# Optimization experiments

Measured on AMD Instinct MI355X. Metric: run time of the kernel, lower is better.

## Reference

```python
import math
import jax, jax.numpy as jnp
import numpy as np

LOG2PI = math.log(2.0 * math.pi)


def setup_inputs() -> dict:
    key = jax.random.key(0)
    k1, k2, k3 = jax.random.split(key, 3)
    N, K, d, l = 16384, 32, 1024, 16
    x = jax.random.normal(k1, (N, d), dtype=jnp.float32)
    MU = jax.random.normal(k2, (K, d), dtype=jnp.float32)
    # modest factor-loading scale so A^T A + s2 I is well conditioned
    A = 0.1 * jax.random.normal(k3, (K, d, l), dtype=jnp.float32)
    log_D = jnp.zeros((K, d), dtype=jnp.float32)       # isotropic sigma^2 = 1
    PI_logits = jnp.zeros((K,), dtype=jnp.float32)     # uniform mixture
    return {"x": x, "MU": MU, "A": A, "log_D": log_D, "PI_logits": PI_logits}


def _responsibilities(x, MU, A, log_D, PI_logits):
    """E-step: faithful vectorization of MFA._component_log_likelihood + softmax.
    Note: the original adds PI (probabilities), not log PI -- kept as-is."""
    K, d, l = A.shape
    PI = jax.nn.softmax(PI_logits)
    iD = jnp.exp(-log_D)                                  # [K,d]
    B = iD[:, :, None] * A                                # iD * A, [K,d,l]
    L = jnp.eye(l, dtype=x.dtype)[None] + jnp.einsum('kdl,kdm->klm', A, B)  # [K,l,l]
    iL = jnp.linalg.inv(L)
    # Mahalanobis distance via Woodbury, without materializing [N,K,d]:
    # term1 = sum_d iD * x_c^2, expanded in x, MU
    sq = (x * x) @ iD.T                                   # [N,K]
    cross = x @ (iD * MU).T                               # [N,K]
    const = jnp.sum(iD * MU * MU, axis=1)                 # [K]
    term1 = sq - 2.0 * cross + const[None, :]
    # term2 = (iD x_c)^T A iL A^T (iD x_c)
    y = jnp.einsum('nd,kdl->nkl', x, B) - jnp.einsum('kd,kdl->kl', MU, B)[None]
    term2 = jnp.einsum('nkl,klm,nkm->nk', y, iL, y)
    m_d = term1 - term2                                   # [N,K]
    log_det_Sigma = jnp.linalg.slogdet(L)[1] - jnp.sum(jnp.log(iD), axis=1)
    comp_LL = PI[None, :] - 0.5 * ((d * LOG2PI + log_det_Sigma)[None, :] + m_d)
    log_r = comp_LL - jax.nn.logsumexp(comp_LL, axis=1, keepdims=True)
    return jnp.exp(log_r)


def reference(x, MU, A, log_D, PI_logits):
    """One EM iteration of MFA.fit: E-step + batched (over K) M-step.
    Returns (MU_new, A_new, log_D_new, PI_logits_new)."""
    K, d, l = A.shape
    r = _responsibilities(x, MU, A, log_D, PI_logits)     # [N,K]
    r_sum = jnp.sum(r, axis=0)                            # [K]
    mu_new = (r.T @ x) / r_sum[:, None]                   # [K,d]
    s2 = jnp.exp(log_D[:, 0])                             # [K]
    eye_l = jnp.eye(l, dtype=x.dtype)
    inv_M = jnp.linalg.inv(jnp.einsum('kdl,kdm->klm', A, A)
                           + s2[:, None, None] * eye_l)   # [K,l,l]
    # SiAi_k = (1/rs_k) * (r_k * x_c)^T @ (x_c @ A_k), expanded so only
    # [N,K,l] (not [N,K,d]) intermediates are built.
    Q = jnp.einsum('nd,kdl->nkl', x, A) - jnp.einsum('kd,kdl->kl', mu_new, A)[None]
    RQ = r[:, :, None] * Q                                # [N,K,l]
    sumRQ = jnp.sum(RQ, axis=0)                           # [K,l]
    SiAi = (jnp.einsum('nd,nkl->kdl', x, RQ)
            - mu_new[:, :, None] * sumRQ[:, None, :]) / r_sum[:, None, None]
    ATSiAi = jnp.einsum('kdl,kdm->klm', A, SiAi)          # [K,l,l]
    invM_AT_Si_Ai = jnp.einsum('klm,kmp->klp', inv_M, ATSiAi)
    A_new = jnp.einsum('kdm,kml->kdl', SiAi,
                       jnp.linalg.inv(s2[:, None, None] * eye_l + invM_AT_Si_Ai))
    SiAi_invM = jnp.einsum('kdm,kml->kdl', SiAi, inv_M)
    t1 = jnp.einsum('kdl,kdl->k', A_new, SiAi_invM)       # trace term
    # trace(S_i) = (sum_n r_nk ||x_n - mu_k||^2) / rs_k, expanded
    x_sq = jnp.sum(x * x, axis=1)                         # [N]
    trace_S = (r.T @ x_sq - r_sum * jnp.sum(mu_new * mu_new, axis=1)) / r_sum
    sigma2_new = (trace_S - t1) / d                       # [K]
    log_D_new = jnp.log(sigma2_new)[:, None] * jnp.ones((1, d), dtype=x.dtype)
    PI_logits_new = jnp.log(r_sum / jnp.sum(r_sum))
    return mu_new, A_new, log_D_new, PI_logits_new
```

## Files before the change

### kernel.cpp

```cpp
#include <hip/hip_runtime.h>
#include <math.h>

#define N_ROWS 16384
#define DIM 1024
#define KC 32
#define LF 16
#define LOG2PI_F 1.8378770664093453f
#define Y_STRIDE 560

typedef __attribute__((ext_vector_type(8))) short bf16x8;
typedef __attribute__((ext_vector_type(4))) float f32x4;

#define O_XH    0
#define O_XL    8388608
#define O_RQT   O_XL
#define O_XBT   16777216
#define O_Y     25165824
#define O_SIAZ  O_Y
#define O_SQ    34340864
#define O_R     34865152
#define O_WETH  35389440
#define O_WETL  35667968
#define O_AQT   35946496
#define O_ID    36208640
#define O_SIAI  36241408
#define O_LMAT  36765696
#define O_M0    36773888
#define O_IL    36782080
#define O_INVM  36790272
#define O_GM    36798464
#define O_IG    36806656
#define O_CB    36814848
#define O_CA    36815360
#define O_CONST 36815872
#define O_SLD   36815904
#define O_LDET  36815936
#define O_PIK   36815968
#define O_CK    36816000
#define O_MUSQ  36816032
#define O_MUACC 36816064
#define O_SUMRQ 36848832
#define O_RSUM  36849344
#define O_RXSQ  36849376
#define O_T1    36849408
#define ZERO_START O_MUACC
#define ZERO_COUNT 33376
#define O_XSQ   36849440

#define OU_MU 0
#define OU_A  32768
#define OU_LD 557056
#define OU_PI 589824

__device__ __forceinline__ ushort f2bf(float f) {
    union { float f; unsigned u; } v; v.f = f;
    unsigned u = v.u;
    return (ushort)((u + 0x7FFFu + ((u >> 16) & 1u)) >> 16);
}
__device__ __forceinline__ float bf2f(ushort b) {
    union { unsigned u; float f; } v; v.u = ((unsigned)b) << 16;
    return v.f;
}

__device__ __forceinline__ float blockReduce256(float v, float* red) {
    int tid = threadIdx.x;
    red[tid] = v; __syncthreads();
    for (int s = 128; s > 0; s >>= 1) {
        if (tid < s) red[tid] += red[tid + s];
        __syncthreads();
    }
    float r = red[0]; __syncthreads();
    return r;
}

__global__ __launch_bounds__(256) void k_conv(const float* __restrict__ x,
    float* __restrict__ ws)
{
    __shared__ ushort tile[64][66];
    int tid = threadIdx.x;
    int n0 = blockIdx.x * 64;
    int row = tid >> 2, seg = tid & 3;
    ushort* xh  = (ushort*)(ws + O_XH);
    ushort* xl  = (ushort*)(ws + O_XL);
    ushort* xbT = (ushort*)(ws + O_XBT);

    for (int c0 = 0; c0 < DIM; c0 += 64) {
        float4 f[4];
        #pragma unroll
        for (int t = 0; t < 4; t++)
            f[t] = *(const float4*)&x[(size_t)(n0 + row)*DIM + c0 + seg*16 + t*4];
        union { ushort u[8]; uint4 v; } ha, hb, la, lb;
        ushort hi16[16];
        #pragma unroll
        for (int e = 0; e < 16; e++) {
            float v = ((const float*)&f[e >> 2])[e & 3];
            ushort h = f2bf(v);
            hi16[e] = h;
            ushort lo = f2bf(v - bf2f(h));
            if (e < 8) { ha.u[e] = h; la.u[e] = lo; }
            else       { hb.u[e-8] = h; lb.u[e-8] = lo; }
        }
        size_t o = (size_t)(n0 + row)*DIM + c0 + seg*16;
        *(uint4*)&xh[o] = ha.v;  *(uint4*)&xh[o + 8] = hb.v;
        *(uint4*)&xl[o] = la.v;  *(uint4*)&xl[o + 8] = lb.v;
        #pragma unroll
        for (int e = 0; e < 16; e++) tile[seg*16 + e][row] = hi16[e];
        __syncthreads();
        int cl = tid >> 2, nseg = tid & 3;
        union { ushort u[8]; uint4 v; } ta, tb;
        #pragma unroll
        for (int e = 0; e < 8; e++) {
            ta.u[e] = tile[cl][nseg*16 + e];
            tb.u[e] = tile[cl][nseg*16 + 8 + e];
        }
        size_t ot = (size_t)(c0 + cl)*N_ROWS + n0 + nseg*16;
        *(uint4*)&xbT[ot] = ta.v; *(uint4*)&xbT[ot + 8] = tb.v;
        __syncthreads();
    }
}

__global__ __launch_bounds__(256) void k_prep(
    const float* __restrict__ MU, const float* __restrict__ A,
    const float* __restrict__ logD, const float* __restrict__ PIl,
    float* __restrict__ ws)
{
    int k = blockIdx.x, tid = threadIdx.x;
    __shared__ float red[256];
    ushort* Weth = (ushort*)(ws + O_WETH);
    ushort* Wetl = (ushort*)(ws + O_WETL);
    ushort* Aqt  = (ushort*)(ws + O_AQT);
    float* iDb = ws + O_ID;

    float cb[LF];
    #pragma unroll
    for (int l = 0; l < LF; l++) cb[l] = 0.f;
    float cst = 0.f, sl = 0.f;

    for (int dd = tid; dd < DIM; dd += 256) {
        float ld  = logD[k*DIM + dd];
        float idv = expf(-ld);
        float mu  = MU[k*DIM + dd];
        cst += idv*mu*mu;
        sl  += ld;
        iDb[(size_t)k*DIM + dd] = idv;
        const float* arow = A + (size_t)(k*DIM + dd)*LF;
        #pragma unroll
        for (int l = 0; l < LF; l++) {
            float a = arow[l];
            float b = idv*a;
            ushort h = f2bf(b);
            Weth[(size_t)(k*LF + l)*DIM + dd] = h;
            Wetl[(size_t)(k*LF + l)*DIM + dd] = f2bf(b - bf2f(h));
            Aqt[(size_t)(k*LF + l)*DIM + dd] = f2bf(a);
            cb[l] += mu*b;
        }
        float cmu = idv*mu;
        ushort hm = f2bf(cmu);
        Weth[(size_t)(512 + k)*DIM + dd] = hm;
        Wetl[(size_t)(512 + k)*DIM + dd] = f2bf(cmu - bf2f(hm));
    }

    for (int l = 0; l < LF; l++) {
        float t = blockReduce256(cb[l], red);
        if (tid == 0) ws[O_CB + k*LF + l] = t;
    }
    {
        float t = blockReduce256(cst, red);
        if (tid == 0) ws[O_CONST + k] = t;
        t = blockReduce256(sl, red);
        if (tid == 0) ws[O_SLD + k] = t;
    }
    if (tid == 0) {
        float mx = -1e30f;
        for (int j = 0; j < KC; j++) mx = fmaxf(mx, PIl[j]);
        float s = 0.f;
        for (int j = 0; j < KC; j++) s += expf(PIl[j] - mx);
        ws[O_PIK + k] = expf(PIl[k] - mx) / s;
    }
    __syncthreads();

    int i = tid >> 4, j = tid & 15;
    float sL = 0.f, sM = 0.f;
    for (int dd = 0; dd < DIM; dd++) {
        const float* arow = A + (size_t)(k*DIM + dd)*LF;
        float ai = arow[i], aj = arow[j];
        float idv = iDb[(size_t)k*DIM + dd];
        sL += ai*aj*idv;
        sM += ai*aj;
    }
    float s2 = expf(logD[k*DIM]);
    ws[O_LMAT + k*256 + tid] = sL + (i == j ? 1.f : 0.f);
    ws[O_M0   + k*256 + tid] = sM + (i == j ? s2  : 0.f);
}

__global__ __launch_bounds__(256) void k_inv16(const float* __restrict__ src,
    float* __restrict__ dst, float* __restrict__ ldet)
{
    __shared__ float M[16][33];
    __shared__ float fac[16];
    __shared__ int spv;
    __shared__ float sld;
    int m = blockIdx.x, tid = threadIdx.x;

    for (int idx = tid; idx < 16*33; idx += 256) {
        int i = idx/33, c = idx%33;
        M[i][c] = (c < 16) ? src[m*256 + i*16 + c]
                           : (c < 32 ? ((i == c-16) ? 1.f : 0.f) : 0.f);
    }
    if (tid == 0) sld = 0.f;
    __syncthreads();

    for (int j = 0; j < 16; j++) {
        if (tid == 0) {
            int p = j; float best = fabsf(M[j][j]);
            for (int i2 = j+1; i2 < 16; i2++) {
                float a = fabsf(M[i2][j]);
                if (a > best) { best = a; p = i2; }
            }
            spv = p;
            sld += logf(fabsf(M[p][j]));
        }
        __syncthreads();
        int p = spv;
        if (p != j && tid < 33) { float t = M[j][tid]; M[j][tid] = M[p][tid]; M[p][tid] = t; }
        __syncthreads();
        float pv = M[j][j];
        __syncthreads();
        if (tid < 33) M[j][tid] = M[j][tid] / pv;
        __syncthreads();
        if (tid < 16) fac[tid] = M[tid][j];
        __syncthreads();
        for (int idx = tid; idx < 16*33; idx += 256) {
            int i2 = idx/33, c = idx%33;
            if (i2 != j) M[i2][c] -= fac[i2]*M[j][c];
        }
        __syncthreads();
    }
    {
        int i = tid >> 4, c = tid & 15;
        dst[m*256 + tid] = M[i][16 + c];
    }
    if (ldet != nullptr && tid == 0) ldet[m] = sld;
}

__global__ void k_prep2(float* __restrict__ ws)
{
    int k = threadIdx.x;
    if (k < KC) {
        ws[O_CK + k] = ws[O_PIK + k]
            - 0.5f*((float)DIM*LOG2PI_F + ws[O_LDET + k] + ws[O_SLD + k] + ws[O_CONST + k]);
    }
}

__global__ __launch_bounds__(256) void k_sq(const float* __restrict__ x,
    const float* __restrict__ iD, float* __restrict__ SQ, float* __restrict__ xsq)
{
    __shared__ float xs[32][65];
    __shared__ float ds[32][65];
    int tid = threadIdx.x;
    int n0 = blockIdx.x * 32;
    int r = tid & 31, ks = (tid >> 5) * 4;
    int srow = tid >> 3, sc = (tid & 7) * 8;
    float acc[4] = {0.f, 0.f, 0.f, 0.f};
    float xsa = 0.f;

    for (int d0 = 0; d0 < DIM; d0 += 64) {
        __syncthreads();
        #pragma unroll
        for (int u = 0; u < 8; u += 4) {
            float4 a = *(const float4*)&x[(size_t)(n0 + srow)*DIM + d0 + sc + u];
            xs[srow][sc+u+0] = a.x*a.x; xs[srow][sc+u+1] = a.y*a.y;
            xs[srow][sc+u+2] = a.z*a.z; xs[srow][sc+u+3] = a.w*a.w;
            float4 b = *(const float4*)&iD[(size_t)srow*DIM + d0 + sc + u];
            ds[srow][sc+u+0] = b.x; ds[srow][sc+u+1] = b.y;
            ds[srow][sc+u+2] = b.z; ds[srow][sc+u+3] = b.w;
        }
        __syncthreads();
        for (int d = 0; d < 64; d++) {
            float xv = xs[r][d];
            if (ks == 0) xsa += xv;
            acc[0] += xv*ds[ks+0][d];
            acc[1] += xv*ds[ks+1][d];
            acc[2] += xv*ds[ks+2][d];
            acc[3] += xv*ds[ks+3][d];
        }
    }
    #pragma unroll
    for (int j = 0; j < 4; j++)
        SQ[(size_t)(n0 + r)*KC + ks + j] = acc[j];
    if (ks == 0) xsq[n0 + r] = xsa;
}

__device__ __forceinline__ void gemm128_core(
    const ushort* __restrict__ Ab, const ushort* __restrict__ Bb,
    size_t Ka, size_t Kb, int m0, int n0, int kbeg, int kend,
    f32x4 acc[4][4])
{
    __shared__ __align__(16) ushort As[2*5120];
    __shared__ __align__(16) ushort Bs[2*5120];
    int tid = threadIdx.x;
    int ar0 = tid >> 2,          ac0 = (tid & 3) * 8;
    int ar1 = (tid + 256) >> 2,  ac1 = ac0;
    int lane = tid & 63, w = tid >> 6;
    int wm = w >> 1, wn = w & 1;
    int lr = lane & 15, lg = lane >> 4;

    float4 ra0, ra1, rb0, rb1;
    auto LOADT = [&](int kt) {
        ra0 = *(const float4*)&Ab[(size_t)(m0 + ar0)*Ka + kt + ac0];
        ra1 = *(const float4*)&Ab[(size_t)(m0 + ar1)*Ka + kt + ac1];
        rb0 = *(const float4*)&Bb[(size_t)(n0 + ar0)*Kb + kt + ac0];
        rb1 = *(const float4*)&Bb[(size_t)(n0 + ar1)*Kb + kt + ac1];
    };
    auto STORET = [&](int buf) {
        *(float4*)&As[buf*5120 + ar0*40 + ac0] = ra0;
        *(float4*)&As[buf*5120 + ar1*40 + ac1] = ra1;
        *(float4*)&Bs[buf*5120 + ar0*40 + ac0] = rb0;
        *(float4*)&Bs[buf*5120 + ar1*40 + ac1] = rb1;
    };

    LOADT(kbeg);
    STORET(0);
    __syncthreads();
    int cur = 0;
    for (int kt = kbeg; kt < kend; kt += 32) {
        bool more = (kt + 32 < kend);
        if (more) LOADT(kt + 32);
        bf16x8 af[4], bfr[4];
        #pragma unroll
        for (int mi = 0; mi < 4; mi++)
            af[mi] = *(bf16x8*)&As[cur*5120 + (wm*64 + mi*16 + lr)*40 + lg*8];
        #pragma unroll
        for (int ni = 0; ni < 4; ni++)
            bfr[ni] = *(bf16x8*)&Bs[cur*5120 + (wn*64 + ni*16 + lr)*40 + lg*8];
        #pragma unroll
        for (int mi = 0; mi < 4; mi++)
            #pragma unroll
            for (int ni = 0; ni < 4; ni++)
                acc[mi][ni] = __builtin_amdgcn_mfma_f32_16x16x32_bf16(
                    af[mi], bfr[ni], acc[mi][ni], 0, 0, 0);
        if (more) STORET(cur ^ 1);
        cur ^= 1;
        __syncthreads();
    }
}

__global__ __launch_bounds__(256) void k_gemm_y(
    const ushort* __restrict__ XH, const ushort* __restrict__ XL,
    const ushort* __restrict__ WH, const ushort* __restrict__ WL,
    float* __restrict__ Y)
{
    int m0 = blockIdx.x * 128, n0 = blockIdx.y * 128;
    f32x4 acc[4][4];
    #pragma unroll
    for (int a = 0; a < 4; a++)
        #pragma unroll
        for (int b = 0; b < 4; b++) acc[a][b] = (f32x4)0.f;
    gemm128_core(XH, WH, DIM, DIM, m0, n0, 0, DIM, acc);
    gemm128_core(XH, WL, DIM, DIM, m0, n0, 0, DIM, acc);
    gemm128_core(XL, WH, DIM, DIM, m0, n0, 0, DIM, acc);
    int lane = threadIdx.x & 63, w = threadIdx.x >> 6;
    int wm = w >> 1, wn = w & 1, lr = lane & 15, lg = lane >> 4;
    #pragma unroll
    for (int mi = 0; mi < 4; mi++)
        #pragma unroll
        for (int ni = 0; ni < 4; ni++) {
            int c = n0 + wn*64 + ni*16 + lr;
            if (c < 544) {
                #pragma unroll
                for (int j = 0; j < 4; j++)
                    Y[(size_t)(m0 + wm*64 + mi*16 + lg*4 + j)*Y_STRIDE + c]
                        = acc[mi][ni][j];
            }
        }
}

__global__ __launch_bounds__(256) void k_gemm_rq(
    const ushort* __restrict__ Ab, const ushort* __restrict__ Bb,
    const float* __restrict__ rr, const float* __restrict__ cA,
    ushort* __restrict__ RQt, float* __restrict__ sumRQ)
{
    __shared__ float rs[128][32];
    __shared__ float cAs[128];
    int tid = threadIdx.x;
    int m0 = blockIdx.x * 128, n0 = blockIdx.y * 128;
    for (int i = tid; i < 128*8; i += 256) {
        int row = i >> 3, kq = (i & 7) * 4;
        *(float4*)&rs[row][kq] = *(const float4*)&rr[(size_t)(m0 + row)*KC + kq];
    }
    if (tid < 128) cAs[tid] = cA[n0 + tid];
    f32x4 acc[4][4];
    #pragma unroll
    for (int a = 0; a < 4; a++)
        #pragma unroll
        for (int b = 0; b < 4; b++) acc[a][b] = (f32x4)0.f;
    gemm128_core(Ab, Bb, DIM, DIM, m0, n0, 0, DIM, acc);
    int lane = tid & 63, w = tid >> 6;
    int wm = w >> 1, wn = w & 1, lr = lane & 15, lg = lane >> 4;
    float colsum[4] = {0.f, 0.f, 0.f, 0.f};
    #pragma unroll
    for (int ni = 0; ni < 4; ni++) {
        int colL = wn*64 + ni*16 + lr;
        int kk = (n0 + colL) >> 4;
        float ca = cAs[colL];
        #pragma unroll
        for (int mi = 0; mi < 4; mi++) {
            int row0 = wm*64 + mi*16 + lg*4;
            union { ushort u[4]; uint2 v; } pk;
            #pragma unroll
            for (int j = 0; j < 4; j++) {
                float rv = rs[row0 + j][kk];
                float q = acc[mi][ni][j] - ca;
                float rq = q * rv;
                colsum[ni] += rq;
                pk.u[j] = f2bf(rq);
            }
            *(uint2*)&RQt[(size_t)(n0 + colL)*N_ROWS + m0 + row0] = pk.v;
        }
    }
    #pragma unroll
    for (int ni = 0; ni < 4; ni++) {
        float v = colsum[ni];
        v += __shfl_xor(v, 16);
        v += __shfl_xor(v, 32);
        if (lg == 0) atomicAdd(&sumRQ[n0 + wn*64 + ni*16 + lr], v);
    }
}

__global__ __launch_bounds__(256) void k_gemm_sz(
    const ushort* __restrict__ Ab, const ushort* __restrict__ Bb,
    float* __restrict__ SiAz)
{
    int m0 = blockIdx.x * 128, n0 = blockIdx.y * 128;
    int kbeg = blockIdx.z * 1024, kend = kbeg + 1024;
    f32x4 acc[4][4];
    #pragma unroll
    for (int a = 0; a < 4; a++)
        #pragma unroll
        for (int b = 0; b < 4; b++) acc[a][b] = (f32x4)0.f;
    gemm128_core(Ab, Bb, N_ROWS, N_ROWS, m0, n0, kbeg, kend, acc);
    float* dst = SiAz + (size_t)blockIdx.z * DIM * 512;
    int lane = threadIdx.x & 63, w = threadIdx.x >> 6;
    int wm = w >> 1, wn = w & 1, lr = lane & 15, lg = lane >> 4;
    #pragma unroll
    for (int mi = 0; mi < 4; mi++)
        #pragma unroll
        for (int ni = 0; ni < 4; ni++) {
            int c = n0 + wn*64 + ni*16 + lr;
            #pragma unroll
            for (int j = 0; j < 4; j++)
                dst[(size_t)(m0 + wm*64 + mi*16 + lg*4 + j)*512 + c] = acc[mi][ni][j];
        }
}

__global__ __launch_bounds__(256) void k_sired(const float* __restrict__ SiAz,
    float* __restrict__ SiAi)
{
    int i = blockIdx.x * 256 + threadIdx.x;
    float s = 0.f;
    #pragma unroll
    for (int z = 0; z < 16; z++) s += SiAz[(size_t)z*DIM*512 + i];
    SiAi[i] = s;
}

__global__ __launch_bounds__(256) void k_epiE(const float* __restrict__ Y,
    const float* __restrict__ SQ, const float* __restrict__ iL,
    const float* __restrict__ cB, const float* __restrict__ Ck,
    const float* __restrict__ xsq,
    float* __restrict__ rr, float* __restrict__ rsum, float* __restrict__ rxsq)
{
    __shared__ float iLs[32*257];
    __shared__ float yr[8*Y_STRIDE];
    __shared__ float cBs[512];
    __shared__ float rs_s[32], rx_s[32];
    int tid = threadIdx.x;
    int n0 = blockIdx.x*8;

    for (int idx = tid; idx < 8192; idx += 256)
        iLs[(idx >> 8)*257 + (idx & 255)] = iL[idx];
    for (int idx = tid; idx < 512; idx += 256) cBs[idx] = cB[idx];
    for (int idx = tid; idx < 8*Y_STRIDE; idx += 256)
        yr[idx] = Y[(size_t)n0*Y_STRIDE + idx];
    if (tid < 32) { rs_s[tid] = 0.f; rx_s[tid] = 0.f; }
    __syncthreads();

    int row = tid >> 5, k = tid & 31;
    const float* yrow = yr + row*Y_STRIDE;
    float y[16];
    #pragma unroll
    for (int j = 0; j < 16; j++) y[j] = yrow[k*16 + j] - cBs[k*16 + j];
    float t2 = 0.f;
    for (int i2 = 0; i2 < 16; i2++) {
        float ti = 0.f;
        const float* ilr = iLs + k*257 + i2*16;
        #pragma unroll
        for (int j = 0; j < 16; j++) ti += ilr[j]*y[j];
        t2 += y[i2]*ti;
    }
    float cross = yrow[512 + k];
    float sq    = SQ[(size_t)(n0 + row)*KC + k];
    float cll = Ck[k] + cross - 0.5f*sq + 0.5f*t2;

    float mx = cll;
    #pragma unroll
    for (int m = 16; m >= 1; m >>= 1) mx = fmaxf(mx, __shfl_xor(mx, m, 32));
    float e = __expf(cll - mx);
    float ssum = e;
    #pragma unroll
    for (int m = 16; m >= 1; m >>= 1) ssum += __shfl_xor(ssum, m, 32);
    float rv = e / ssum;

    rr[(size_t)(n0 + row)*KC + k] = rv;
    atomicAdd(&rs_s[k], rv);
    atomicAdd(&rx_s[k], rv*xsq[n0 + row]);
    __syncthreads();
    if (tid < 32) {
        atomicAdd(&rsum[tid], rs_s[tid]);
        atomicAdd(&rxsq[tid], rx_s[tid]);
    }
}

__global__ __launch_bounds__(256) void k_mu(const float* __restrict__ x,
    const float* __restrict__ rr, float* __restrict__ muacc)
{
    __shared__ float rl[8][32];
    int tid = threadIdx.x;
    int d0 = blockIdx.x*128;
    int n0 = blockIdx.y*512;
    int dd = d0 + (tid & 127);
    int kg = (tid >> 7)*16;
    float acc[16];
    #pragma unroll
    for (int j = 0; j < 16; j++) acc[j] = 0.f;

    for (int nb = 0; nb < 512; nb += 8) {
        __syncthreads();
        rl[tid >> 5][tid & 31] = rr[(size_t)(n0 + nb + (tid >> 5))*KC + (tid & 31)];
        __syncthreads();
        for (int r2 = 0; r2 < 8; r2++) {
            float xv = x[(size_t)(n0 + nb + r2)*DIM + dd];
            #pragma unroll
            for (int j = 0; j < 16; j++) acc[j] += rl[r2][kg + j]*xv;
        }
    }
    #pragma unroll
    for (int j = 0; j < 16; j++)
        atomicAdd(&muacc[(size_t)(kg + j)*DIM + dd], acc[j]);
}

__global__ __launch_bounds__(256) void k_mufin(const float* __restrict__ muacc,
    const float* __restrict__ rsum, const float* __restrict__ A,
    float* __restrict__ out_mu, float* __restrict__ cA, float* __restrict__ musq)
{
    __shared__ float red[256];
    int k = blockIdx.x, tid = threadIdx.x;
    float rs = rsum[k];
    float ca[16];
    #pragma unroll
    for (int l = 0; l < 16; l++) ca[l] = 0.f;
    float msq = 0.f;
    for (int dd = tid; dd < DIM; dd += 256) {
        float m = muacc[(size_t)k*DIM + dd] / rs;
        out_mu[(size_t)k*DIM + dd] = m;
        msq += m*m;
        const float* arow = A + (size_t)(k*DIM + dd)*LF;
        #pragma unroll
        for (int l = 0; l < 16; l++) ca[l] += m*arow[l];
    }
    for (int l = 0; l < 16; l++) {
        float t = blockReduce256(ca[l], red);
        if (tid == 0) cA[k*16 + l] = t;
    }
    float t = blockReduce256(msq, red);
    if (tid == 0) musq[k] = t;
}

__global__ __launch_bounds__(256) void k_ats(const float* __restrict__ A,
    const float* __restrict__ logD, const float* __restrict__ SiAi,
    const float* __restrict__ cA, const float* __restrict__ sumRQ,
    const float* __restrict__ rsum, const float* __restrict__ invM,
    float* __restrict__ Gm)
{
    __shared__ float atsl[256];
    int k = blockIdx.x, tid = threadIdx.x, i = tid >> 4, j = tid & 15;
    float s = 0.f;
    for (int dd = 0; dd < DIM; dd++) {
        s += A[((size_t)k*DIM + dd)*LF + i] * SiAi[(size_t)dd*512 + k*16 + j];
    }
    float av = (s - cA[k*16 + i]*sumRQ[k*16 + j]) / rsum[k];
    atsl[tid] = av;
    __syncthreads();
    float s2 = expf(logD[k*DIM]);
    float g = (i == j) ? s2 : 0.f;
    #pragma unroll
    for (int m = 0; m < 16; m++) g += invM[k*256 + i*16 + m]*atsl[m*16 + j];
    Gm[k*256 + tid] = g;
}

__global__ __launch_bounds__(256) void k_anew(const float* __restrict__ SiAi,
    const float* __restrict__ mu_out, const float* __restrict__ sumRQ,
    const float* __restrict__ rsum, const float* __restrict__ iG,
    const float* __restrict__ invM, float* __restrict__ outA, float* __restrict__ t1)
{
    __shared__ float iGs[256], iMs[256];
    __shared__ float red[256];
    int k = blockIdx.x, tid = threadIdx.x;
    int dd = blockIdx.y*256 + tid;
    iGs[tid] = iG[k*256 + tid];
    iMs[tid] = invM[k*256 + tid];
    __syncthreads();
    float rs = rsum[k];
    float mv = mu_out[(size_t)k*DIM + dd];
    float sr[16];
    #pragma unroll
    for (int j = 0; j < 16; j++)
        sr[j] = (SiAi[(size_t)dd*512 + k*16 + j] - mv*sumRQ[k*16 + j]) / rs;
    float t1p = 0.f;
    float an[16];
    #pragma unroll
    for (int j = 0; j < 16; j++) {
        float a = 0.f, b = 0.f;
        #pragma unroll
        for (int m = 0; m < 16; m++) {
            a += sr[m]*iGs[m*16 + j];
            b += sr[m]*iMs[m*16 + j];
        }
        an[j] = a;
        t1p += a*b;
    }
    #pragma unroll
    for (int j = 0; j < 16; j += 4)
        *(float4*)&outA[((size_t)k*DIM + dd)*LF + j] =
            make_float4(an[j], an[j+1], an[j+2], an[j+3]);
    red[tid] = t1p; __syncthreads();
    for (int s = 128; s > 0; s >>= 1) {
        if (tid < s) red[tid] += red[tid + s];
        __syncthreads();
    }
    if (tid == 0) atomicAdd(&t1[k], red[0]);
}

__global__ __launch_bounds__(256) void k_final(const float* __restrict__ rsum,
    const float* __restrict__ rxsq, const float* __restrict__ musq,
    const float* __restrict__ t1, float* __restrict__ out)
{
    int k = blockIdx.x, tid = threadIdx.x;
    float rs = rsum[k];
    float ts = (rxsq[k] - rs*musq[k]) / rs;
    float sig = (ts - t1[k]) / (float)DIM;
    float ld = logf(sig);
    for (int dd = tid; dd < DIM; dd += 256)
        out[OU_LD + (size_t)k*DIM + dd] = ld;
    if (tid == 0) {
        float s = 0.f;
        for (int j = 0; j < KC; j++) s += rsum[j];
        out[OU_PI + k] = logf(rs / s);
    }
}

extern "C" void kernel_launch(void* const* d_in, const int* in_sizes, int n_in,
                              void* d_out, int out_size, void* d_ws, size_t ws_size,
                              hipStream_t stream) {
    const float* x    = (const float*)d_in[0];
    const float* MU   = (const float*)d_in[1];
    const float* A    = (const float*)d_in[2];
    const float* logD = (const float*)d_in[3];
    const float* PIl  = (const float*)d_in[4];
    float* out = (float*)d_out;
    float* ws  = (float*)d_ws;

    hipMemsetAsync(ws + ZERO_START, 0, (size_t)ZERO_COUNT*sizeof(float), stream);

    k_conv<<<N_ROWS/64, 256, 0, stream>>>(x, ws);
    k_prep<<<KC, 256, 0, stream>>>(MU, A, logD, PIl, ws);
    k_inv16<<<KC, 256, 0, stream>>>(ws + O_LMAT, ws + O_IL, ws + O_LDET);
    k_inv16<<<KC, 256, 0, stream>>>(ws + O_M0, ws + O_INVM, nullptr);
    k_prep2<<<1, 32, 0, stream>>>(ws);
    k_sq<<<N_ROWS/32, 256, 0, stream>>>(x, ws + O_ID, ws + O_SQ, ws + O_XSQ);

    k_gemm_y<<<dim3(N_ROWS/128, 5), 256, 0, stream>>>(
        (const ushort*)(ws + O_XH), (const ushort*)(ws + O_XL),
        (const ushort*)(ws + O_WETH), (const ushort*)(ws + O_WETL),
        ws + O_Y);

    k_epiE<<<N_ROWS/8, 256, 0, stream>>>(ws + O_Y, ws + O_SQ, ws + O_IL,
                                         ws + O_CB, ws + O_CK, ws + O_XSQ,
                                         ws + O_R, ws + O_RSUM, ws + O_RXSQ);

    k_mu<<<dim3(8, 32), 256, 0, stream>>>(x, ws + O_R, ws + O_MUACC);
    k_mufin<<<KC, 256, 0, stream>>>(ws + O_MUACC, ws + O_RSUM, A,
                                    out + OU_MU, ws + O_CA, ws + O_MUSQ);

    k_gemm_rq<<<dim3(N_ROWS/128, 4), 256, 0, stream>>>(
        (const ushort*)(ws + O_XH), (const ushort*)(ws + O_AQT),
        ws + O_R, ws + O_CA, (ushort*)(ws + O_RQT), ws + O_SUMRQ);

    k_gemm_sz<<<dim3(8, 4, 16), 256, 0, stream>>>(
        (const ushort*)(ws + O_XBT), (const ushort*)(ws + O_RQT), ws + O_SIAZ);
    k_sired<<<DIM*512/256, 256, 0, stream>>>(ws + O_SIAZ, ws + O_SIAI);

    k_ats<<<KC, 256, 0, stream>>>(A, logD, ws + O_SIAI, ws + O_CA, ws + O_SUMRQ,
                                  ws + O_RSUM, ws + O_INVM, ws + O_GM);
    k_inv16<<<KC, 256, 0, stream>>>(ws + O_GM, ws + O_IG, nullptr);
    k_anew<<<dim3(KC, 4), 256, 0, stream>>>(ws + O_SIAI, out + OU_MU, ws + O_SUMRQ,
                                            ws + O_RSUM, ws + O_IG, ws + O_INVM,
                                            out + OU_A, ws + O_T1);
    k_final<<<KC, 256, 0, stream>>>(ws + O_RSUM, ws + O_RXSQ, ws + O_MUSQ,
                                    ws + O_T1, out);
}
```

Before: 670.6 us.

## Split E-step GEMM into fused 3-pass MFMA kernel plus aux cross/sq GEMM

Replaces the three-pass gemm_y (which re-read X via gemm128_core three times and padded to 5 column tiles) with a single-loop kernel computing hi*hi + lo*hi + hi*lo MFMAs on 4 column tiles. The cross term and the scalar fp32 k_sq sq term move to a new MFMA kernel using a bf16 x^2 array produced in k_conv, which also now computes ||x||^2. The epilogue processes 32 rows per block reading Y directly with vector loads, and the A^T SiAi reduction is split over d with atomics for more parallelism. This adds an extra bf16 x^2 buffer write and lowers sq precision to single bf16.

```diff
diff --git a/kernel.cpp b/kernel.cpp
--- a/kernel.cpp
+++ b/kernel.cpp
@@ -6,7 +6,6 @@
 #define KC 32
 #define LF 16
 #define LOG2PI_F 1.8378770664093453f
-#define Y_STRIDE 560
 
 typedef __attribute__((ext_vector_type(8))) short bf16x8;
 typedef __attribute__((ext_vector_type(4))) float f32x4;
@@ -14,38 +13,43 @@
 #define O_XH    0
 #define O_XL    8388608
 #define O_RQT   O_XL
-#define O_XBT   16777216
-#define O_Y     25165824
+#define O_X2H   16777216
+#define O_XBT   25165824
+#define O_Y     33554432
 #define O_SIAZ  O_Y
-#define O_SQ    34340864
-#define O_R     34865152
-#define O_WETH  35389440
-#define O_WETL  35667968
-#define O_AQT   35946496
-#define O_ID    36208640
-#define O_SIAI  36241408
-#define O_LMAT  36765696
-#define O_M0    36773888
-#define O_IL    36782080
-#define O_INVM  36790272
-#define O_GM    36798464
-#define O_IG    36806656
-#define O_CB    36814848
-#define O_CA    36815360
-#define O_CONST 36815872
-#define O_SLD   36815904
-#define O_LDET  36815936
-#define O_PIK   36815968
-#define O_CK    36816000
-#define O_MUSQ  36816032
-#define O_MUACC 36816064
-#define O_SUMRQ 36848832
-#define O_RSUM  36849344
-#define O_RXSQ  36849376
-#define O_T1    36849408
+#define O_AUX   41943040
+#define O_SIAI  O_AUX
+#define O_R     42991616
+#define O_WETH  43515904
+#define O_WETL  43778048
+#define O_CRH   44040192
+#define O_CRL   44056576
+#define O_IDC   44072960
+#define O_AQT   44089344
+#define O_ID    44351488
+#define O_LMAT  44384256
+#define O_M0    44392448
+#define O_IL    44400640
+#define O_INVM  44408832
+#define O_GM    44417024
+#define O_IG    44425216
+#define O_CB    44433408
+#define O_CA    44433920
+#define O_CONST 44434432
+#define O_SLD   44434464
+#define O_LDET  44434496
+#define O_PIK   44434528
+#define O_CK    44434560
+#define O_MUSQ  44434592
+#define O_MUACC 44434624
+#define O_SUMRQ 44467392
+#define O_RSUM  44467904
+#define O_RXSQ  44467936
+#define O_T1    44467968
+#define O_ATS   44468000
 #define ZERO_START O_MUACC
-#define ZERO_COUNT 33376
-#define O_XSQ   36849440
+#define ZERO_COUNT 41568
+#define O_XSQ   44476192
 
 #define OU_MU 0
 #define OU_A  32768
@@ -82,27 +86,32 @@
     int row = tid >> 2, seg = tid & 3;
     ushort* xh  = (ushort*)(ws + O_XH);
     ushort* xl  = (ushort*)(ws + O_XL);
+    ushort* x2h = (ushort*)(ws + O_X2H);
     ushort* xbT = (ushort*)(ws + O_XBT);
+    float xs_acc = 0.f;
 
     for (int c0 = 0; c0 < DIM; c0 += 64) {
         float4 f[4];
         #pragma unroll
         for (int t = 0; t < 4; t++)
             f[t] = *(const float4*)&x[(size_t)(n0 + row)*DIM + c0 + seg*16 + t*4];
-        union { ushort u[8]; uint4 v; } ha, hb, la, lb;
+        union { ushort u[8]; uint4 v; } ha, hb, la, lb, qa, qb;
         ushort hi16[16];
         #pragma unroll
         for (int e = 0; e < 16; e++) {
             float v = ((const float*)&f[e >> 2])[e & 3];
+            xs_acc += v*v;
             ushort h = f2bf(v);
             hi16[e] = h;
             ushort lo = f2bf(v - bf2f(h));
-            if (e < 8) { ha.u[e] = h; la.u[e] = lo; }
-            else       { hb.u[e-8] = h; lb.u[e-8] = lo; }
+            ushort q  = f2bf(v*v);
+            if (e < 8) { ha.u[e] = h; la.u[e] = lo; qa.u[e] = q; }
+            else       { hb.u[e-8] = h; lb.u[e-8] = lo; qb.u[e-8] = q; }
         }
         size_t o = (size_t)(n0 + row)*DIM + c0 + seg*16;
-        *(uint4*)&xh[o] = ha.v;  *(uint4*)&xh[o + 8] = hb.v;
-        *(uint4*)&xl[o] = la.v;  *(uint4*)&xl[o + 8] = lb.v;
+        *(uint4*)&xh[o] = ha.v;   *(uint4*)&xh[o + 8] = hb.v;
+        *(uint4*)&xl[o] = la.v;   *(uint4*)&xl[o + 8] = lb.v;
+        *(uint4*)&x2h[o] = qa.v;  *(uint4*)&x2h[o + 8] = qb.v;
         #pragma unroll
         for (int e = 0; e < 16; e++) tile[seg*16 + e][row] = hi16[e];
         __syncthreads();
@@ -117,6 +126,9 @@
         *(uint4*)&xbT[ot] = ta.v; *(uint4*)&xbT[ot + 8] = tb.v;
         __syncthreads();
     }
+    xs_acc += __shfl_xor(xs_acc, 1);
+    xs_acc += __shfl_xor(xs_acc, 2);
+    if ((tid & 3) == 0) (ws + O_XSQ)[n0 + row] = xs_acc;
 }
 
 __global__ __launch_bounds__(256) void k_prep(
@@ -128,6 +140,9 @@
     __shared__ float red[256];
     ushort* Weth = (ushort*)(ws + O_WETH);
     ushort* Wetl = (ushort*)(ws + O_WETL);
+    ushort* Crh  = (ushort*)(ws + O_CRH);
+    ushort* Crl  = (ushort*)(ws + O_CRL);
+    ushort* Idc  = (ushort*)(ws + O_IDC);
     ushort* Aqt  = (ushort*)(ws + O_AQT);
     float* iDb = ws + O_ID;
 
@@ -156,8 +171,9 @@
         }
         float cmu = idv*mu;
         ushort hm = f2bf(cmu);
-        Weth[(size_t)(512 + k)*DIM + dd] = hm;
-        Wetl[(size_t)(512 + k)*DIM + dd] = f2bf(cmu - bf2f(hm));
+        Crh[(size_t)k*DIM + dd] = hm;
+        Crl[(size_t)k*DIM + dd] = f2bf(cmu - bf2f(hm));
+        Idc[(size_t)k*DIM + dd] = f2bf(idv);
     }
 
     for (int l = 0; l < LF; l++) {
@@ -252,43 +268,145 @@
     }
 }
 
-__global__ __launch_bounds__(256) void k_sq(const float* __restrict__ x,
-    const float* __restrict__ iD, float* __restrict__ SQ, float* __restrict__ xsq)
-{
-    __shared__ float xs[32][65];
-    __shared__ float ds[32][65];
+__global__ __launch_bounds__(256) void k_g1f(
+    const ushort* __restrict__ XH, const ushort* __restrict__ XL,
+    const ushort* __restrict__ WH, const ushort* __restrict__ WL,
+    float* __restrict__ Y)
+{
+    __shared__ __align__(16) ushort sXH[5120], sXL[5120], sWH[5120], sWL[5120];
     int tid = threadIdx.x;
-    int n0 = blockIdx.x * 32;
-    int r = tid & 31, ks = (tid >> 5) * 4;
-    int srow = tid >> 3, sc = (tid & 7) * 8;
-    float acc[4] = {0.f, 0.f, 0.f, 0.f};
-    float xsa = 0.f;
-
-    for (int d0 = 0; d0 < DIM; d0 += 64) {
-        __syncthreads();
-        #pragma unroll
-        for (int u = 0; u < 8; u += 4) {
-            float4 a = *(const float4*)&x[(size_t)(n0 + srow)*DIM + d0 + sc + u];
-            xs[srow][sc+u+0] = a.x*a.x; xs[srow][sc+u+1] = a.y*a.y;
-            xs[srow][sc+u+2] = a.z*a.z; xs[srow][sc+u+3] = a.w*a.w;
-            float4 b = *(const float4*)&iD[(size_t)srow*DIM + d0 + sc + u];
-            ds[srow][sc+u+0] = b.x; ds[srow][sc+u+1] = b.y;
-            ds[srow][sc+u+2] = b.z; ds[srow][sc+u+3] = b.w;
-        }
-        __syncthreads();
-        for (int d = 0; d < 64; d++) {
-            float xv = xs[r][d];
-            if (ks == 0) xsa += xv;
-            acc[0] += xv*ds[ks+0][d];
-            acc[1] += xv*ds[ks+1][d];
-            acc[2] += xv*ds[ks+2][d];
-            acc[3] += xv*ds[ks+3][d];
-        }
-    }
-    #pragma unroll
-    for (int j = 0; j < 4; j++)
-        SQ[(size_t)(n0 + r)*KC + ks + j] = acc[j];
-    if (ks == 0) xsq[n0 + r] = xsa;
+    int m0 = blockIdx.x*128, n0 = blockIdx.y*128;
+    int ar0 = tid >> 2, ac0 = (tid & 3)*8;
+    int ar1 = ar0 + 64;
+    int lane = tid & 63, w = tid >> 6;
+    int wm = w >> 1, wn = w & 1, lr = lane & 15, lg = lane >> 4;
+
+    f32x4 acc[4][4];
+    #pragma unroll
+    for (int a = 0; a < 4; a++)
+        #pragma unroll
+        for (int b = 0; b < 4; b++) acc[a][b] = (f32x4)0.f;
+
+    float4 rxh0, rxh1, rxl0, rxl1, rwh0, rwh1, rwl0, rwl1;
+    auto LOADT = [&](int kt) {
+        rxh0 = *(const float4*)&XH[(size_t)(m0 + ar0)*DIM + kt + ac0];
+        rxh1 = *(const float4*)&XH[(size_t)(m0 + ar1)*DIM + kt + ac0];
+        rxl0 = *(const float4*)&XL[(size_t)(m0 + ar0)*DIM + kt + ac0];
+        rxl1 = *(const float4*)&XL[(size_t)(m0 + ar1)*DIM + kt + ac0];
+        rwh0 = *(const float4*)&WH[(size_t)(n0 + ar0)*DIM + kt + ac0];
+        rwh1 = *(const float4*)&WH[(size_t)(n0 + ar1)*DIM + kt + ac0];
+        rwl0 = *(const float4*)&WL[(size_t)(n0 + ar0)*DIM + kt + ac0];
+        rwl1 = *(const float4*)&WL[(size_t)(n0 + ar1)*DIM + kt + ac0];
+    };
+
+    LOADT(0);
+    for (int kt = 0; kt < DIM; kt += 32) {
+        __syncthreads();
+        *(float4*)&sXH[ar0*40 + ac0] = rxh0; *(float4*)&sXH[ar1*40 + ac0] = rxh1;
+        *(float4*)&sXL[ar0*40 + ac0] = rxl0; *(float4*)&sXL[ar1*40 + ac0] = rxl1;
+        *(float4*)&sWH[ar0*40 + ac0] = rwh0; *(float4*)&sWH[ar1*40 + ac0] = rwh1;
+        *(float4*)&sWL[ar0*40 + ac0] = rwl0; *(float4*)&sWL[ar1*40 + ac0] = rwl1;
+        if (kt + 32 < DIM) LOADT(kt + 32);
+        __syncthreads();
+
+        bf16x8 bwh[4], bwl[4];
+        #pragma unroll
+        for (int ni = 0; ni < 4; ni++) {
+            bwh[ni] = *(bf16x8*)&sWH[(wn*64 + ni*16 + lr)*40 + lg*8];
+            bwl[ni] = *(bf16x8*)&sWL[(wn*64 + ni*16 + lr)*40 + lg*8];
+        }
+        #pragma unroll
+        for (int mi = 0; mi < 4; mi++) {
+            bf16x8 axh = *(bf16x8*)&sXH[(wm*64 + mi*16 + lr)*40 + lg*8];
+            bf16x8 axl = *(bf16x8*)&sXL[(wm*64 + mi*16 + lr)*40 + lg*8];
+            #pragma unroll
+            for (int ni = 0; ni < 4; ni++) {
+                acc[mi][ni] = __builtin_amdgcn_mfma_f32_16x16x32_bf16(axh, bwh[ni], acc[mi][ni], 0, 0, 0);
+                acc[mi][ni] = __builtin_amdgcn_mfma_f32_16x16x32_bf16(axl, bwh[ni], acc[mi][ni], 0, 0, 0);
+                acc[mi][ni] = __builtin_amdgcn_mfma_f32_16x16x32_bf16(axh, bwl[ni], acc[mi][ni], 0, 0, 0);
+            }
+        }
+    }
+    #pragma unroll
+    for (int mi = 0; mi < 4; mi++)
+        #pragma unroll
+        for (int ni = 0; ni < 4; ni++) {
+            int c = n0 + wn*64 + ni*16 + lr;
+            #pragma unroll
+            for (int j = 0; j < 4; j++)
+                Y[(size_t)(m0 + wm*64 + mi*16 + lg*4 + j)*512 + c] = acc[mi][ni][j];
+        }
+}
+
+__global__ __launch_bounds__(256) void k_aux(
+    const ushort* __restrict__ XH, const ushort* __restrict__ XL,
+    const ushort* __restrict__ X2, const ushort* __restrict__ CRH,
+    const ushort* __restrict__ CRL, const ushort* __restrict__ IDC,
+    float* __restrict__ AUX)
+{
+    __shared__ __align__(16) ushort sXH[5120], sXL[5120], sX2[5120];
+    __shared__ __align__(16) ushort sB[3840];
+    int tid = threadIdx.x;
+    int m0 = blockIdx.x*128;
+    int lane = tid & 63, w = tid >> 6;
+    int lr = lane & 15, lg = lane >> 4;
+
+    f32x4 acc[2][4];
+    #pragma unroll
+    for (int a = 0; a < 2; a++)
+        #pragma unroll
+        for (int b = 0; b < 4; b++) acc[a][b] = (f32x4)0.f;
+
+    for (int kt = 0; kt < DIM; kt += 32) {
+        __syncthreads();
+        #pragma unroll
+        for (int t = 0; t < 2; t++) {
+            int idx = tid + t*256;
+            int row = idx >> 2, seg = (idx & 3)*8;
+            *(float4*)&sXH[row*40 + seg] = *(const float4*)&XH[(size_t)(m0 + row)*DIM + kt + seg];
+            *(float4*)&sXL[row*40 + seg] = *(const float4*)&XL[(size_t)(m0 + row)*DIM + kt + seg];
+            *(float4*)&sX2[row*40 + seg] = *(const float4*)&X2[(size_t)(m0 + row)*DIM + kt + seg];
+        }
+        for (int idx = tid; idx < 384; idx += 256) {
+            int row = idx >> 2, seg = (idx & 3)*8;
+            const ushort* src = (row < 32) ? &CRH[(size_t)row*DIM + kt + seg]
+                              : (row < 64) ? &CRL[(size_t)(row-32)*DIM + kt + seg]
+                                           : &IDC[(size_t)(row-64)*DIM + kt + seg];
+            *(float4*)&sB[row*40 + seg] = *(const float4*)src;
+        }
+        __syncthreads();
+
+        bf16x8 bch[2], bcl[2], bd[2];
+        #pragma unroll
+        for (int cf = 0; cf < 2; cf++) {
+            bch[cf] = *(bf16x8*)&sB[(cf*16 + lr)*40 + lg*8];
+            bcl[cf] = *(bf16x8*)&sB[(32 + cf*16 + lr)*40 + lg*8];
+            bd[cf]  = *(bf16x8*)&sB[(64 + cf*16 + lr)*40 + lg*8];
+        }
+        #pragma unroll
+        for (int rf = 0; rf < 2; rf++) {
+            int rbase = (w*32 + rf*16 + lr)*40 + lg*8;
+            bf16x8 axh = *(bf16x8*)&sXH[rbase];
+            bf16x8 axl = *(bf16x8*)&sXL[rbase];
+            bf16x8 ax2 = *(bf16x8*)&sX2[rbase];
+            #pragma unroll
+            for (int cf = 0; cf < 2; cf++) {
+                acc[rf][cf] = __builtin_amdgcn_mfma_f32_16x16x32_bf16(axh, bch[cf], acc[rf][cf], 0, 0, 0);
+                acc[rf][cf] = __builtin_amdgcn_mfma_f32_16x16x32_bf16(axl, bch[cf], acc[rf][cf], 0, 0, 0);
+                acc[rf][cf] = __builtin_amdgcn_mfma_f32_16x16x32_bf16(axh, bcl[cf], acc[rf][cf], 0, 0, 0);
+                acc[rf][2+cf] = __builtin_amdgcn_mfma_f32_16x16x32_bf16(ax2, bd[cf], acc[rf][2+cf], 0, 0, 0);
+            }
+        }
+    }
+    #pragma unroll
+    for (int rf = 0; rf < 2; rf++)
+        #pragma unroll
+        for (int cf = 0; cf < 4; cf++) {
+            int col = cf*16 + lr;
+            #pragma unroll
+            for (int j = 0; j < 4; j++)
+                AUX[(size_t)(m0 + w*32 + rf*16 + lg*4 + j)*64 + col] = acc[rf][cf][j];
+        }
 }
 
 __device__ __forceinline__ void gemm128_core(
@@ -345,36 +463,6 @@
     }
 }
 
-__global__ __launch_bounds__(256) void k_gemm_y(
-    const ushort* __restrict__ XH, const ushort* __restrict__ XL,
-    const ushort* __restrict__ WH, const ushort* __restrict__ WL,
-    float* __restrict__ Y)
-{
-    int m0 = blockIdx.x * 128, n0 = blockIdx.y * 128;
-    f32x4 acc[4][4];
-    #pragma unroll
-    for (int a = 0; a < 4; a++)
-        #pragma unroll
-        for (int b = 0; b < 4; b++) acc[a][b] = (f32x4)0.f;
-    gemm128_core(XH, WH, DIM, DIM, m0, n0, 0, DIM, acc);
-    gemm128_core(XH, WL, DIM, DIM, m0, n0, 0, DIM, acc);
-    gemm128_core(XL, WH, DIM, DIM, m0, n0, 0, DIM, acc);
-    int lane = threadIdx.x & 63, w = threadIdx.x >> 6;
-    int wm = w >> 1, wn = w & 1, lr = lane & 15, lg = lane >> 4;
-    #pragma unroll
-    for (int mi = 0; mi < 4; mi++)
-        #pragma unroll
-        for (int ni = 0; ni < 4; ni++) {
-            int c = n0 + wn*64 + ni*16 + lr;
-            if (c < 544) {
-                #pragma unroll
-                for (int j = 0; j < 4; j++)
-                    Y[(size_t)(m0 + wm*64 + mi*16 + lg*4 + j)*Y_STRIDE + c]
-                        = acc[mi][ni][j];
-            }
-        }
-}
-
 __global__ __launch_bounds__(256) void k_gemm_rq(
     const ushort* __restrict__ Ab, const ushort* __restrict__ Bb,
     const float* __restrict__ rr, const float* __restrict__ cA,
@@ -464,55 +552,66 @@
 }
 
 __global__ __launch_bounds__(256) void k_epiE(const float* __restrict__ Y,
-    const float* __restrict__ SQ, const float* __restrict__ iL,
+    const float* __restrict__ AUX, const float* __restrict__ iL,
     const float* __restrict__ cB, const float* __restrict__ Ck,
     const float* __restrict__ xsq,
     float* __restrict__ rr, float* __restrict__ rsum, float* __restrict__ rxsq)
 {
-    __shared__ float iLs[32*257];
-    __shared__ float yr[8*Y_STRIDE];
+    __shared__ __align__(16) float iLs[32*260];
     __shared__ float cBs[512];
     __shared__ float rs_s[32], rx_s[32];
     int tid = threadIdx.x;
-    int n0 = blockIdx.x*8;
+    int n0 = blockIdx.x*32;
 
     for (int idx = tid; idx < 8192; idx += 256)
-        iLs[(idx >> 8)*257 + (idx & 255)] = iL[idx];
+        iLs[(idx >> 8)*260 + (idx & 255)] = iL[idx];
     for (int idx = tid; idx < 512; idx += 256) cBs[idx] = cB[idx];
-    for (int idx = tid; idx < 8*Y_STRIDE; idx += 256)
-        yr[idx] = Y[(size_t)n0*Y_STRIDE + idx];
     if (tid < 32) { rs_s[tid] = 0.f; rx_s[tid] = 0.f; }
     __syncthreads();
 
-    int row = tid >> 5, k = tid & 31;
-    const float* yrow = yr + row*Y_STRIDE;
-    float y[16];
-    #pragma unroll
-    for (int j = 0; j < 16; j++) y[j] = yrow[k*16 + j] - cBs[k*16 + j];
-    float t2 = 0.f;
-    for (int i2 = 0; i2 < 16; i2++) {
-        float ti = 0.f;
-        const float* ilr = iLs + k*257 + i2*16;
-        #pragma unroll
-        for (int j = 0; j < 16; j++) ti += ilr[j]*y[j];
-        t2 += y[i2]*ti;
-    }
-    float cross = yrow[512 + k];
-    float sq    = SQ[(size_t)(n0 + row)*KC + k];
-    float cll = Ck[k] + cross - 0.5f*sq + 0.5f*t2;
-
-    float mx = cll;
-    #pragma unroll
-    for (int m = 16; m >= 1; m >>= 1) mx = fmaxf(mx, __shfl_xor(mx, m, 32));
-    float e = __expf(cll - mx);
-    float ssum = e;
-    #pragma unroll
-    for (int m = 16; m >= 1; m >>= 1) ssum += __shfl_xor(ssum, m, 32);
-    float rv = e / ssum;
-
-    rr[(size_t)(n0 + row)*KC + k] = rv;
-    atomicAdd(&rs_s[k], rv);
-    atomicAdd(&rx_s[k], rv*xsq[n0 + row]);
+    int row8 = tid >> 5, k = tid & 31;
+    const float* ilr = iLs + k*260;
+    float ck = Ck[k];
+
+    for (int it = 0; it < 4; it++) {
+        int n = n0 + it*8 + row8;
+        float y[16];
+        #pragma unroll
+        for (int j = 0; j < 16; j += 4) {
+            float4 v = *(const float4*)&Y[(size_t)n*512 + k*16 + j];
+            y[j] = v.x - cBs[k*16 + j];     y[j+1] = v.y - cBs[k*16 + j+1];
+            y[j+2] = v.z - cBs[k*16 + j+2]; y[j+3] = v.w - cBs[k*16 + j+3];
+        }
+        float t2 = 0.f;
+        #pragma unroll
+        for (int i2 = 0; i2 < 16; i2++) {
+            float4 a = *(const float4*)&ilr[i2*16];
+            float4 b = *(const float4*)&ilr[i2*16 + 4];
+            float4 c = *(const float4*)&ilr[i2*16 + 8];
+            float4 d = *(const float4*)&ilr[i2*16 + 12];
+            float ti = a.x*y[0] + a.y*y[1] + a.z*y[2] + a.w*y[3]
+                     + b.x*y[4] + b.y*y[5] + b.z*y[6] + b.w*y[7]
+                     + c.x*y[8] + c.y*y[9] + c.z*y[10] + c.w*y[11]
+                     + d.x*y[12] + d.y*y[13] + d.z*y[14] + d.w*y[15];
+            t2 += y[i2]*ti;
+        }
+        float cross = AUX[(size_t)n*64 + k];
+        float sq    = AUX[(size_t)n*64 + 32 + k];
+        float cll = ck + cross - 0.5f*sq + 0.5f*t2;
+
+        float mx = cll;
+        #pragma unroll
+        for (int m = 16; m >= 1; m >>= 1) mx = fmaxf(mx, __shfl_xor(mx, m, 32));
+        float e = __expf(cll - mx);
+        float ssum = e;
+        #pragma unroll
+        for (int m = 16; m >= 1; m >>= 1) ssum += __shfl_xor(ssum, m, 32);
+        float rv = e / ssum;
+
+        rr[(size_t)n*KC + k] = rv;
+        atomicAdd(&rs_s[k], rv);
+        atomicAdd(&rx_s[k], rv*xsq[n]);
+    }
     __syncthreads();
     if (tid < 32) {
         atomicAdd(&rsum[tid], rs_s[tid]);
@@ -575,19 +674,26 @@
     if (tid == 0) musq[k] = t;
 }
 
-__global__ __launch_bounds__(256) void k_ats(const float* __restrict__ A,
-    const float* __restrict__ logD, const float* __restrict__ SiAi,
-    const float* __restrict__ cA, const float* __restrict__ sumRQ,
-    const float* __restrict__ rsum, const float* __restrict__ invM,
-    float* __restrict__ Gm)
+__global__ __launch_bounds__(256) void k_ats1(const float* __restrict__ A,
+    const float* __restrict__ SiAi, float* __restrict__ ATS)
+{
+    int k = blockIdx.x, tid = threadIdx.x, i = tid >> 4, j = tid & 15;
+    int d0 = blockIdx.y*128;
+    float s = 0.f;
+    #pragma unroll 4
+    for (int dd = d0; dd < d0 + 128; dd++)
+        s += A[((size_t)k*DIM + dd)*LF + i] * SiAi[(size_t)dd*512 + k*16 + j];
+    atomicAdd(&ATS[k*256 + tid], s);
+}
+
+__global__ __launch_bounds__(256) void k_ats2(const float* __restrict__ ATS,
+    const float* __restrict__ logD, const float* __restrict__ cA,
+    const float* __restrict__ sumRQ, const float* __restrict__ rsum,
+    const float* __restrict__ invM, float* __restrict__ Gm)
 {
     __shared__ float atsl[256];
     int k = blockIdx.x, tid = threadIdx.x, i = tid >> 4, j = tid & 15;
-    float s = 0.f;
-    for (int dd = 0; dd < DIM; dd++) {
-        s += A[((size_t)k*DIM + dd)*LF + i] * SiAi[(size_t)dd*512 + k*16 + j];
-    }
-    float av = (s - cA[k*16 + i]*sumRQ[k*16 + j]) / rsum[k];
+    float av = (ATS[k*256 + tid] - cA[k*16 + i]*sumRQ[k*16 + j]) / rsum[k];
     atsl[tid] = av;
     __syncthreads();
     float s2 = expf(logD[k*DIM]);
@@ -676,16 +782,20 @@
     k_inv16<<<KC, 256, 0, stream>>>(ws + O_LMAT, ws + O_IL, ws + O_LDET);
     k_inv16<<<KC, 256, 0, stream>>>(ws + O_M0, ws + O_INVM, nullptr);
     k_prep2<<<1, 32, 0, stream>>>(ws);
-    k_sq<<<N_ROWS/32, 256, 0, stream>>>(x, ws + O_ID, ws + O_SQ, ws + O_XSQ);
-
-    k_gemm_y<<<dim3(N_ROWS/128, 5), 256, 0, stream>>>(
+
+    k_g1f<<<dim3(N_ROWS/128, 4), 256, 0, stream>>>(
         (const ushort*)(ws + O_XH), (const ushort*)(ws + O_XL),
         (const ushort*)(ws + O_WETH), (const ushort*)(ws + O_WETL),
         ws + O_Y);
-
-    k_epiE<<<N_ROWS/8, 256, 0, stream>>>(ws + O_Y, ws + O_SQ, ws + O_IL,
-                                         ws + O_CB, ws + O_CK, ws + O_XSQ,
-                                         ws + O_R, ws + O_RSUM, ws + O_RXSQ);
+    k_aux<<<N_ROWS/128, 256, 0, stream>>>(
+        (const ushort*)(ws + O_XH), (const ushort*)(ws + O_XL),
+        (const ushort*)(ws + O_X2H), (const ushort*)(ws + O_CRH),
+        (const ushort*)(ws + O_CRL), (const ushort*)(ws + O_IDC),
+        ws + O_AUX);
+
+    k_epiE<<<N_ROWS/32, 256, 0, stream>>>(ws + O_Y, ws + O_AUX, ws + O_IL,
+                                          ws + O_CB, ws + O_CK, ws + O_XSQ,
+                                          ws + O_R, ws + O_RSUM, ws + O_RXSQ);
 
     k_mu<<<dim3(8, 32), 256, 0, stream>>>(x, ws + O_R, ws + O_MUACC);
     k_mufin<<<KC, 256, 0, stream>>>(ws + O_MUACC, ws + O_RSUM, A,
@@ -696,11 +806,12 @@
         ws + O_R, ws + O_CA, (ushort*)(ws + O_RQT), ws + O_SUMRQ);
 
     k_gemm_sz<<<dim3(8, 4, 16), 256, 0, stream>>>(
-        (const ushort*)(ws + O_XBT), (const ushort*)(ws + O_RQT), ws + O_SIAZ);
-    k_sired<<<DIM*512/256, 256, 0, stream>>>(ws + O_SIAZ, ws + O_SIAI);
-
-    k_ats<<<KC, 256, 0, stream>>>(A, logD, ws + O_SIAI, ws + O_CA, ws + O_SUMRQ,
-                                  ws + O_RSUM, ws + O_INVM, ws + O_GM);
+        (const ushort*)(ws + O_XBT), (const ushort*)(ws + O_RQT), ws + O_Y);
+    k_sired<<<DIM*512/256, 256, 0, stream>>>(ws + O_Y, ws + O_SIAI);
+
+    k_ats1<<<dim3(KC, 8), 256, 0, stream>>>(A, ws + O_SIAI, ws + O_ATS);
+    k_ats2<<<KC, 256, 0, stream>>>(ws + O_ATS, logD, ws + O_CA, ws + O_SUMRQ,
+                                   ws + O_RSUM, ws + O_INVM, ws + O_GM);
     k_inv16<<<KC, 256, 0, stream>>>(ws + O_GM, ws + O_IG, nullptr);
     k_anew<<<dim3(KC, 4), 256, 0, stream>>>(ws + O_SIAI, out + OU_MU, ws + O_SUMRQ,
                                             ws + O_RSUM, ws + O_IG, ws + O_INVM,
```

New measurement: 570.4 us. 1.18x faster.
